# Optimization experiments

Hardware: AMD Instinct MI355X
Metric: run time of the kernel (lower is better)

The kernel has to match this reference:

```python
import jax, jax.numpy as jnp
import numpy as np

B, P, E, H = 16, 1024, 1024, 16
DH = E // H  # 64


def setup_inputs() -> dict:
    key = jax.random.key(0)
    ks = jax.random.split(key, 7)
    # kaiming_uniform on [H, DH, DH]: bound = sqrt(6 / fan_in), fan_in = DH
    bound = float(np.sqrt(6.0 / DH))
    w_att_val = jax.random.uniform(ks[0], (H, DH, DH), jnp.float32, -bound, bound)
    attention_bias = jax.random.normal(ks[1], (H, P, P), jnp.float32)
    lb = float(1.0 / np.sqrt(E))
    wv_w = jax.random.uniform(ks[2], (E, E), jnp.float32, -lb, lb)
    wv_b = jax.random.uniform(ks[3], (E,), jnp.float32, -lb, lb)
    out_w = jax.random.uniform(ks[4], (E, E), jnp.float32, -lb, lb)
    out_b = jax.random.uniform(ks[5], (E,), jnp.float32, -lb, lb)
    x = jax.random.normal(ks[6], (B, P, E), jnp.float32)
    return {"x": x, "w_att_val": w_att_val, "attention_bias": attention_bias,
            "wv_w": wv_w, "wv_b": wv_b, "out_w": out_w, "out_b": out_b}


def reference(x, w_att_val, attention_bias, wv_w, wv_b, out_w, out_b):
    b, p, e = x.shape
    dh = e // H
    # split heads: [B, H, P, DH]
    x_h = x.reshape(b, p, H, dh).transpose(0, 2, 1, 3)
    # bilinear scores: (x_h @ W) @ x_h^T -> [B, H, P, P]
    xw = jnp.einsum('bhpd,hde->bhpe', x_h, w_att_val)
    scores = jnp.einsum('bhpe,bhqe->bhpq', xw, x_h)
    scores = scores / jnp.sqrt(jnp.asarray(dh, x.dtype)) + attention_bias
    attn = jax.nn.softmax(scores, axis=-1)
    # values: Linear(E, E) then split heads
    vx = x @ wv_w.T + wv_b
    vx = vx.reshape(b, p, H, dh).transpose(0, 2, 1, 3)
    out = jnp.einsum('bhpq,bhqd->bhpd', attn, vx)
    out = out.transpose(0, 2, 1, 3).reshape(b, p, e)
    return out @ out_w.T + out_b
```

## Files before the change

### kernel.cpp

```cpp
#include <hip/hip_runtime.h>

#define PB 16
#define PP 1024
#define PE 1024
#define PH 16
#define PDH 64

typedef __attribute__((ext_vector_type(8))) short bf16x8;
typedef __attribute__((ext_vector_type(4))) short bf16x4;
typedef __attribute__((ext_vector_type(4))) float f32x4;

#define LOG2E 1.44269504088896340736f

__device__ __forceinline__ short f2bf(float f) {
    union { float f; unsigned u; } a;
    a.f = f;
    unsigned u = a.u;
    u += 0x7fffu + ((u >> 16) & 1u);
    return (short)(u >> 16);
}
__device__ __forceinline__ float bf2f(short s) {
    union { unsigned u; float f; } a;
    a.u = ((unsigned)(unsigned short)s) << 16;
    return a.f;
}
__device__ __forceinline__ unsigned cvtpk(float lo, float hi) {
    unsigned r;
    asm("v_cvt_pk_bf16_f32 %0, %1, %2" : "=v"(r) : "v"(lo), "v"(hi));
    return r;
}
union U8 { unsigned u[4]; bf16x8 v; };
__device__ __forceinline__ void async16(const void* g, void* l) {
    __builtin_amdgcn_global_load_lds(
        (const __attribute__((address_space(1))) unsigned int*)g,
        (__attribute__((address_space(3))) unsigned int*)l, 16, 0, 0);
}

__global__ __launch_bounds__(256) void wconv(const float* __restrict__ wvw,
                                             const float* __restrict__ outw,
                                             short* __restrict__ wvwb,
                                             short* __restrict__ outwb) {
    int bid = blockIdx.x;
    const float* src = (bid < 512) ? wvw : outw;
    short* dst = (bid < 512) ? wvwb : outwb;
    int lb = (bid < 512) ? bid : bid - 512;
    size_t idx = ((size_t)lb * 256 + threadIdx.x) * 8;
    float4 a = *(const float4*)(src + idx);
    float4 b = *(const float4*)(src + idx + 4);
    bf16x8 t = {f2bf(a.x), f2bf(a.y), f2bf(a.z), f2bf(a.w),
                f2bf(b.x), f2bf(b.y), f2bf(b.z), f2bf(b.w)};
    *(bf16x8*)(dst + idx) = t;
}

__global__ __launch_bounds__(256) void xw_kernel(const float* __restrict__ x,
                                                 const float* __restrict__ watt,
                                                 short* __restrict__ xw,
                                                 short* __restrict__ xbf) {
    int bid = blockIdx.x;
    int q4 = bid & 3;
    int bh = bid >> 2;
    int h = bh & 15;
    __shared__ short Wt[64][88];

    int tid = threadIdx.x;
    {
        const float* W = watt + (size_t)h * 4096;
        int idx = tid * 16;
        int d = idx >> 6, e0 = idx & 63;
#pragma unroll
        for (int i = 0; i < 16; i += 4) {
            float4 v = *(const float4*)(W + d * 64 + e0 + i);
            Wt[e0 + i + 0][d] = f2bf(v.x);
            Wt[e0 + i + 1][d] = f2bf(v.y);
            Wt[e0 + i + 2][d] = f2bf(v.z);
            Wt[e0 + i + 3][d] = f2bf(v.w);
        }
    }
    __syncthreads();

    int wave = tid >> 6, lane = tid & 63;
    int lm = lane & 15, lq = lane >> 4;

    bf16x8 bfr[4][2];
#pragma unroll
    for (int nt = 0; nt < 4; nt++)
#pragma unroll
        for (int kf = 0; kf < 2; kf++)
            bfr[nt][kf] = *(const bf16x8*)&Wt[nt * 16 + lm][kf * 32 + lq * 8];

    int b = bh >> 4;
    const float QSCALE = 0.125f * LOG2E;
    for (int pass = 0; pass < 4; pass++) {
        int p0 = q4 * 256 + pass * 64 + wave * 16;
        const float* xrow = x + ((size_t)(b * 1024 + p0 + lm)) * 1024 + h * 64;
        short* xorow = xbf + ((size_t)(b * 1024 + p0 + lm)) * 1024 + h * 64;
        bf16x8 af[2];
#pragma unroll
        for (int kf = 0; kf < 2; kf++) {
            float4 v0 = *(const float4*)(xrow + kf * 32 + lq * 8);
            float4 v1 = *(const float4*)(xrow + kf * 32 + lq * 8 + 4);
            bf16x8 t;
            t[0] = f2bf(v0.x); t[1] = f2bf(v0.y); t[2] = f2bf(v0.z); t[3] = f2bf(v0.w);
            t[4] = f2bf(v1.x); t[5] = f2bf(v1.y); t[6] = f2bf(v1.z); t[7] = f2bf(v1.w);
            af[kf] = t;
            *(bf16x8*)(xorow + kf * 32 + lq * 8) = t;
        }
#pragma unroll
        for (int nt = 0; nt < 4; nt++) {
            f32x4 acc = {0.f, 0.f, 0.f, 0.f};
            acc = __builtin_amdgcn_mfma_f32_16x16x32_bf16(af[0], bfr[nt][0], acc, 0, 0, 0);
            acc = __builtin_amdgcn_mfma_f32_16x16x32_bf16(af[1], bfr[nt][1], acc, 0, 0, 0);
            size_t base = ((size_t)bh * 1024 + p0 + lq * 4) * 64 + nt * 16 + lm;
#pragma unroll
            for (int r = 0; r < 4; r++)
                xw[base + (size_t)r * 64] = f2bf(acc[r] * QSCALE);
        }
    }
}

__global__ __launch_bounds__(256) void vx_gemm(const short* __restrict__ xbf,
                                               const short* __restrict__ wvwb,
                                               const float* __restrict__ wvb,
                                               short* __restrict__ vt) {
    int logical = (blockIdx.x & 7) * 128 + (blockIdx.x >> 3);
    int mblk = logical >> 3, nblk = logical & 7;
    int m0 = mblk * 128, n0 = nblk * 128;
    __shared__ short As[128 * 32];
    __shared__ short Bs[128 * 32];

    int tid = threadIdx.x;
    int wv = tid >> 6, ln = tid & 63;
    int c0 = wv * 2;
    int rrow = ln >> 2, rseg = (ln & 3) * 8;
    const short* gA = xbf + (size_t)(m0 + c0 * 16 + rrow) * 1024 + rseg;
    const short* gB = wvwb + (size_t)(n0 + c0 * 16 + rrow) * 1024 + rseg;
    short* lA = As + c0 * 512;
    short* lB = Bs + c0 * 512;

    int lane = ln, lm = lane & 15, lq = lane >> 4;
    int wm = (wv >> 1) * 64, wn = (wv & 1) * 64;

    f32x4 acc[4][4];
#pragma unroll
    for (int i = 0; i < 4; i++)
#pragma unroll
        for (int j = 0; j < 4; j++) acc[i][j] = (f32x4){0.f, 0.f, 0.f, 0.f};

    for (int k0 = 0; k0 < 1024; k0 += 32) {
        __syncthreads();
        async16(gA + k0, lA);
        async16(gA + k0 + 16 * 1024, lA + 512);
        async16(gB + k0, lB);
        async16(gB + k0 + 16 * 1024, lB + 512);
        __syncthreads();
        bf16x8 af[4], bfr[4];
#pragma unroll
        for (int mt = 0; mt < 4; mt++) af[mt] = *(const bf16x8*)&As[(wm + mt * 16 + lm) * 32 + lq * 8];
#pragma unroll
        for (int nt = 0; nt < 4; nt++) bfr[nt] = *(const bf16x8*)&Bs[(wn + nt * 16 + lm) * 32 + lq * 8];
#pragma unroll
        for (int mt = 0; mt < 4; mt++)
#pragma unroll
            for (int nt = 0; nt < 4; nt++)
                acc[mt][nt] = __builtin_amdgcn_mfma_f32_16x16x32_bf16(af[mt], bfr[nt], acc[mt][nt], 0, 0, 0);
    }

#pragma unroll
    for (int nt = 0; nt < 4; nt++) {
        int e = n0 + wn + nt * 16 + lm;
        float bias = wvb[e];
        int hh = e >> 6, dd = e & 63;
#pragma unroll
        for (int mt = 0; mt < 4; mt++) {
            int pg = m0 + wm + mt * 16 + lq * 4;
            int bb = pg >> 10, pp = pg & 1023;
            bf16x4 pk;
#pragma unroll
            for (int r = 0; r < 4; r++) pk[r] = f2bf(acc[mt][nt][r] + bias);
            *(bf16x4*)(vt + ((size_t)((bb * 16 + hh) * 64 + dd)) * 1024 + pp) = pk;
        }
    }
}

__global__ __launch_bounds__(256, 3) void flash_kernel(const short* __restrict__ xbf,
                                                       const short* __restrict__ xw,
                                                       const short* __restrict__ vt,
                                                       const float* __restrict__ bias,
                                                       short* __restrict__ obuf) {
    int logical = (blockIdx.x & 7) * 256 + (blockIdx.x >> 3);
    int qblk = logical & 7, b = (logical >> 3) & 15, h = logical >> 7;
    int bh = b * 16 + h;
    int q0 = qblk * 128;

    __shared__ short Ks[64][72];
    __shared__ short Vs[64][72];
    __shared__ float Rs[4][36];

    int tid = threadIdx.x, wave = tid >> 6, lane = tid & 63;
    int lm = lane & 15, lq = lane >> 4;

    bf16x8 qa[2][2];
#pragma unroll
    for (int qt = 0; qt < 2; qt++)
#pragma unroll
        for (int kf = 0; kf < 2; kf++)
            qa[qt][kf] = *(const bf16x8*)(xw + ((size_t)bh * 1024 + q0 + wave * 32 + qt * 16 + lm) * 64 + kf * 32 + lq * 8);

    f32x4 o[2][4];
#pragma unroll
    for (int qt = 0; qt < 2; qt++)
#pragma unroll
        for (int dt = 0; dt < 4; dt++) o[qt][dt] = (f32x4){0.f, 0.f, 0.f, 0.f};
    float rs[2] = {0.f, 0.f};

    int ci0 = tid * 2, ci1 = tid * 2 + 1;
    int r0 = ci0 >> 3, s0 = (ci0 & 7) * 8;
    int r1 = ci1 >> 3, s1 = (ci1 & 7) * 8;
    const short* kg = xbf + ((size_t)(b * 1024)) * 1024 + h * 64;
    const short* vg = vt + ((size_t)bh * 64) * 1024;
    const float* bg = bias + ((size_t)h << 20) + (size_t)(q0 + wave * 32) * 1024;

    bf16x8 kr[2], vr[2];
    float4 br[4][2];
    kr[0] = *(const bf16x8*)(kg + (size_t)r0 * 1024 + s0);
    kr[1] = *(const bf16x8*)(kg + (size_t)r1 * 1024 + s1);
    vr[0] = *(const bf16x8*)(vg + (size_t)r0 * 1024 + s0);
    vr[1] = *(const bf16x8*)(vg + (size_t)r1 * 1024 + s1);
#pragma unroll
    for (int kt = 0; kt < 4; kt++)
#pragma unroll
        for (int qt = 0; qt < 2; qt++)
            br[kt][qt] = *(const float4*)(bg + (size_t)(qt * 16 + lm) * 1024 + kt * 16 + lq * 4);
    *(bf16x8*)&Ks[r0][s0] = kr[0];
    *(bf16x8*)&Ks[r1][s1] = kr[1];
    *(bf16x8*)&Vs[r0][s0] = vr[0];
    *(bf16x8*)&Vs[r1][s1] = vr[1];

    for (int tile = 0; tile < 16; tile++) {
        int kv0 = tile * 64;
        __syncthreads();

        f32x4 s[4][2];
#pragma unroll
        for (int kt = 0; kt < 4; kt++)
#pragma unroll
            for (int qt = 0; qt < 2; qt++) {
                float4 bv = br[kt][qt];
                s[kt][qt] = (f32x4){bv.x * LOG2E, bv.y * LOG2E, bv.z * LOG2E, bv.w * LOG2E};
            }

        if (tile < 15) {
            int kvn = kv0 + 64;
            kr[0] = *(const bf16x8*)(kg + (size_t)(kvn + r0) * 1024 + s0);
            kr[1] = *(const bf16x8*)(kg + (size_t)(kvn + r1) * 1024 + s1);
            vr[0] = *(const bf16x8*)(vg + (size_t)r0 * 1024 + kvn + s0);
            vr[1] = *(const bf16x8*)(vg + (size_t)r1 * 1024 + kvn + s1);
#pragma unroll
            for (int kt = 0; kt < 4; kt++)
#pragma unroll
                for (int qt = 0; qt < 2; qt++)
                    br[kt][qt] = *(const float4*)(bg + (size_t)(qt * 16 + lm) * 1024 + kvn + kt * 16 + lq * 4);
        }

        __builtin_amdgcn_s_setprio(1);
#pragma unroll
        for (int kf = 0; kf < 2; kf++) {
            bf16x8 ka[4];
#pragma unroll
            for (int kt = 0; kt < 4; kt++)
                ka[kt] = *(const bf16x8*)&Ks[kt * 16 + lm][kf * 32 + lq * 8];
#pragma unroll
            for (int kt = 0; kt < 4; kt++)
#pragma unroll
                for (int qt = 0; qt < 2; qt++)
                    s[kt][qt] = __builtin_amdgcn_mfma_f32_16x16x32_bf16(ka[kt], qa[qt][kf], s[kt][qt], 0, 0, 0);
        }
        __builtin_amdgcn_s_setprio(0);

#pragma unroll
        for (int kt = 0; kt < 4; kt++)
#pragma unroll
            for (int qt = 0; qt < 2; qt++)
#pragma unroll
                for (int r = 0; r < 4; r++) {
                    float pv = __builtin_amdgcn_exp2f(s[kt][qt][r]);
                    s[kt][qt][r] = pv;
                    rs[qt] += pv;
                }

        __builtin_amdgcn_s_setprio(1);
#pragma unroll
        for (int kf = 0; kf < 2; kf++) {
            bf16x8 pa[2];
#pragma unroll
            for (int qt = 0; qt < 2; qt++) {
                U8 u;
                u.u[0] = cvtpk(s[kf * 2][qt][0], s[kf * 2][qt][1]);
                u.u[1] = cvtpk(s[kf * 2][qt][2], s[kf * 2][qt][3]);
                u.u[2] = cvtpk(s[kf * 2 + 1][qt][0], s[kf * 2 + 1][qt][1]);
                u.u[3] = cvtpk(s[kf * 2 + 1][qt][2], s[kf * 2 + 1][qt][3]);
                pa[qt] = u.v;
            }
#pragma unroll
            for (int dt = 0; dt < 4; dt++) {
                U8 uv;
                *(bf16x4*)&uv.u[0] = *(const bf16x4*)&Vs[dt * 16 + lm][kf * 32 + lq * 4];
                *(bf16x4*)&uv.u[2] = *(const bf16x4*)&Vs[dt * 16 + lm][kf * 32 + 16 + lq * 4];
#pragma unroll
                for (int qt = 0; qt < 2; qt++)
                    o[qt][dt] = __builtin_amdgcn_mfma_f32_16x16x32_bf16(pa[qt], uv.v, o[qt][dt], 0, 0, 0);
            }
        }
        __builtin_amdgcn_s_setprio(0);

        __syncthreads();
        if (tile < 15) {
            *(bf16x8*)&Ks[r0][s0] = kr[0];
            *(bf16x8*)&Ks[r1][s1] = kr[1];
            *(bf16x8*)&Vs[r0][s0] = vr[0];
            *(bf16x8*)&Vs[r1][s1] = vr[1];
        }
    }

#pragma unroll
    for (int qt = 0; qt < 2; qt++) {
        rs[qt] += __shfl_xor(rs[qt], 16);
        rs[qt] += __shfl_xor(rs[qt], 32);
    }
    if (lq == 0) { Rs[wave][lm] = rs[0]; Rs[wave][16 + lm] = rs[1]; }
    __syncthreads();

#pragma unroll
    for (int qt = 0; qt < 2; qt++) {
        float inv[4];
#pragma unroll
        for (int r = 0; r < 4; r++)
            inv[r] = 1.f / Rs[wave][qt * 16 + lq * 4 + r];
#pragma unroll
        for (int dt = 0; dt < 4; dt++) {
            int e = h * 64 + dt * 16 + lm;
#pragma unroll
            for (int r = 0; r < 4; r++) {
                int p = q0 + wave * 32 + qt * 16 + lq * 4 + r;
                obuf[((size_t)(b * 1024 + p)) * 1024 + e] = f2bf(o[qt][dt][r] * inv[r]);
            }
        }
    }
}

__global__ __launch_bounds__(256) void out_gemm(const short* __restrict__ obuf,
                                                const short* __restrict__ outwb,
                                                const float* __restrict__ outb,
                                                float* __restrict__ out) {
    int logical = (blockIdx.x & 7) * 128 + (blockIdx.x >> 3);
    int mblk = logical >> 3, nblk = logical & 7;
    int m0 = mblk * 128, n0 = nblk * 128;
    __shared__ short As[128 * 32];
    __shared__ short Bs[128 * 32];

    int tid = threadIdx.x;
    int wv = tid >> 6, ln = tid & 63;
    int c0 = wv * 2;
    int rrow = ln >> 2, rseg = (ln & 3) * 8;
    const short* gA = obuf + (size_t)(m0 + c0 * 16 + rrow) * 1024 + rseg;
    const short* gB = outwb + (size_t)(n0 + c0 * 16 + rrow) * 1024 + rseg;
    short* lA = As + c0 * 512;
    short* lB = Bs + c0 * 512;

    int lm = ln & 15, lq = ln >> 4;
    int wm = (wv >> 1) * 64, wn = (wv & 1) * 64;

    f32x4 acc[4][4];
#pragma unroll
    for (int i = 0; i < 4; i++)
#pragma unroll
        for (int j = 0; j < 4; j++) acc[i][j] = (f32x4){0.f, 0.f, 0.f, 0.f};

    for (int k0 = 0; k0 < 1024; k0 += 32) {
        __syncthreads();
        async16(gA + k0, lA);
        async16(gA + k0 + 16 * 1024, lA + 512);
        async16(gB + k0, lB);
        async16(gB + k0 + 16 * 1024, lB + 512);
        __syncthreads();
        bf16x8 af[4], bfr[4];
#pragma unroll
        for (int mt = 0; mt < 4; mt++) af[mt] = *(const bf16x8*)&As[(wm + mt * 16 + lm) * 32 + lq * 8];
#pragma unroll
        for (int nt = 0; nt < 4; nt++) bfr[nt] = *(const bf16x8*)&Bs[(wn + nt * 16 + lm) * 32 + lq * 8];
#pragma unroll
        for (int mt = 0; mt < 4; mt++)
#pragma unroll
            for (int nt = 0; nt < 4; nt++)
                acc[mt][nt] = __builtin_amdgcn_mfma_f32_16x16x32_bf16(af[mt], bfr[nt], acc[mt][nt], 0, 0, 0);
    }

#pragma unroll
    for (int nt = 0; nt < 4; nt++) {
        int e = n0 + wn + nt * 16 + lm;
        float bias = outb[e];
#pragma unroll
        for (int mt = 0; mt < 4; mt++) {
            int pg = m0 + wm + mt * 16 + lq * 4;
#pragma unroll
            for (int r = 0; r < 4; r++)
                out[(size_t)(pg + r) * 1024 + e] = acc[mt][nt][r] + bias;
        }
    }
}

extern "C" void kernel_launch(void* const* d_in, const int* in_sizes, int n_in,
                              void* d_out, int out_size, void* d_ws, size_t ws_size,
                              hipStream_t stream) {
    const float* x    = (const float*)d_in[0];
    const float* watt = (const float*)d_in[1];
    const float* bias = (const float*)d_in[2];
    const float* wvw  = (const float*)d_in[3];
    const float* wvb  = (const float*)d_in[4];
    const float* outw = (const float*)d_in[5];
    const float* outb = (const float*)d_in[6];
    float* out = (float*)d_out;

    char* ws = (char*)d_ws;
    short* xw     = (short*)ws;
    short* vt     = (short*)(ws + ((size_t)32 << 20));
    short* obuf   = (short*)(ws + ((size_t)64 << 20));
    short* xbf    = (short*)(ws + ((size_t)96 << 20));
    short* wvwb   = (short*)(ws + ((size_t)128 << 20));
    short* outwb  = (short*)(ws + ((size_t)130 << 20));

    xw_kernel<<<PB * PH * 4, 256, 0, stream>>>(x, watt, xw, xbf);
    wconv<<<1024, 256, 0, stream>>>(wvw, outw, wvwb, outwb);
    vx_gemm<<<(PB * PP / 128) * (PE / 128), 256, 0, stream>>>(xbf, wvwb, wvb, vt);
    flash_kernel<<<PB * PH * (PP / 128), 256, 0, stream>>>(xbf, xw, vt, bias, obuf);
    out_gemm<<<(PB * PP / 128) * (PE / 128), 256, 0, stream>>>(obuf, outwb, outb, out);
}
```

Baseline: 423.2 us.

## Pre-pack attention bias to bf16 in MFMA fragment layout for flash kernel

```diff
diff --git a/kernel.cpp b/kernel.cpp
--- a/kernel.cpp
+++ b/kernel.cpp
@@ -34,6 +34,37 @@
     __builtin_amdgcn_global_load_lds(
         (const __attribute__((address_space(1))) unsigned int*)g,
         (__attribute__((address_space(3))) unsigned int*)l, 16, 0, 0);
+}
+
+__global__ __launch_bounds__(256) void bias_prep(const float* __restrict__ bias,
+                                                 short* __restrict__ biasP) {
+    int bid = blockIdx.x;
+    int h = bid >> 7, qblk = (bid >> 4) & 7, tile = bid & 15;
+    int q0 = qblk * 128, kv0 = tile * 64;
+    __shared__ short T[128][68];
+
+    int t = threadIdx.x;
+    {
+        int qr = t >> 1, half = t & 1;
+        const float* src = bias + ((size_t)h << 20) + (size_t)(q0 + qr) * 1024 + kv0 + half * 32;
+#pragma unroll
+        for (int i = 0; i < 32; i += 4) {
+            float4 v = *(const float4*)(src + i);
+            bf16x4 p = {f2bf(v.x * LOG2E), f2bf(v.y * LOG2E), f2bf(v.z * LOG2E), f2bf(v.w * LOG2E)};
+            *(bf16x4*)&T[qr][half * 32 + i] = p;
+        }
+    }
+    __syncthreads();
+
+    int w = t >> 6, l = t & 63, lm = l & 15, lq = l >> 4;
+    short* dst = biasP + (((size_t)(h * 16 + tile) * 8 + qblk) * 4 + w) * 2048 + l * 8;
+#pragma unroll
+    for (int j = 0; j < 4; j++) {
+        bf16x4 a = *(const bf16x4*)&T[w * 32 + lm][j * 16 + lq * 4];
+        bf16x4 b = *(const bf16x4*)&T[w * 32 + 16 + lm][j * 16 + lq * 4];
+        bf16x8 o = {a[0], a[1], a[2], a[3], b[0], b[1], b[2], b[3]};
+        *(bf16x8*)(dst + j * 512) = o;
+    }
 }
 
 __global__ __launch_bounds__(256) void wconv(const float* __restrict__ wvw,
@@ -185,7 +216,7 @@
 __global__ __launch_bounds__(256, 3) void flash_kernel(const short* __restrict__ xbf,
                                                        const short* __restrict__ xw,
                                                        const short* __restrict__ vt,
-                                                       const float* __restrict__ bias,
+                                                       const short* __restrict__ biasP,
                                                        short* __restrict__ obuf) {
     int logical = (blockIdx.x & 7) * 256 + (blockIdx.x >> 3);
     int qblk = logical & 7, b = (logical >> 3) & 15, h = logical >> 7;
@@ -218,19 +249,18 @@
     int r1 = ci1 >> 3, s1 = (ci1 & 7) * 8;
     const short* kg = xbf + ((size_t)(b * 1024)) * 1024 + h * 64;
     const short* vg = vt + ((size_t)bh * 64) * 1024;
-    const float* bg = bias + ((size_t)h << 20) + (size_t)(q0 + wave * 32) * 1024;
+    const short* bg = biasP + (((size_t)(h * 16) * 8 + qblk) * 4 + wave) * 2048 + lane * 8;
+    const size_t BT_STRIDE = 65536;
 
     bf16x8 kr[2], vr[2];
-    float4 br[4][2];
+    bf16x8 br[4];
     kr[0] = *(const bf16x8*)(kg + (size_t)r0 * 1024 + s0);
     kr[1] = *(const bf16x8*)(kg + (size_t)r1 * 1024 + s1);
     vr[0] = *(const bf16x8*)(vg + (size_t)r0 * 1024 + s0);
     vr[1] = *(const bf16x8*)(vg + (size_t)r1 * 1024 + s1);
 #pragma unroll
     for (int kt = 0; kt < 4; kt++)
-#pragma unroll
-        for (int qt = 0; qt < 2; qt++)
-            br[kt][qt] = *(const float4*)(bg + (size_t)(qt * 16 + lm) * 1024 + kt * 16 + lq * 4);
+        br[kt] = *(const bf16x8*)(bg + kt * 512);
     *(bf16x8*)&Ks[r0][s0] = kr[0];
     *(bf16x8*)&Ks[r1][s1] = kr[1];
     *(bf16x8*)&Vs[r0][s0] = vr[0];
@@ -245,8 +275,8 @@
         for (int kt = 0; kt < 4; kt++)
 #pragma unroll
             for (int qt = 0; qt < 2; qt++) {
-                float4 bv = br[kt][qt];
-                s[kt][qt] = (f32x4){bv.x * LOG2E, bv.y * LOG2E, bv.z * LOG2E, bv.w * LOG2E};
+                s[kt][qt] = (f32x4){bf2f(br[kt][qt * 4 + 0]), bf2f(br[kt][qt * 4 + 1]),
+                                    bf2f(br[kt][qt * 4 + 2]), bf2f(br[kt][qt * 4 + 3])};
             }
 
         if (tile < 15) {
@@ -255,14 +285,12 @@
             kr[1] = *(const bf16x8*)(kg + (size_t)(kvn + r1) * 1024 + s1);
             vr[0] = *(const bf16x8*)(vg + (size_t)r0 * 1024 + kvn + s0);
             vr[1] = *(const bf16x8*)(vg + (size_t)r1 * 1024 + kvn + s1);
+            const short* bgn = bg + (size_t)(tile + 1) * BT_STRIDE;
 #pragma unroll
             for (int kt = 0; kt < 4; kt++)
-#pragma unroll
-                for (int qt = 0; qt < 2; qt++)
-                    br[kt][qt] = *(const float4*)(bg + (size_t)(qt * 16 + lm) * 1024 + kvn + kt * 16 + lq * 4);
-        }
-
-        __builtin_amdgcn_s_setprio(1);
+                br[kt] = *(const bf16x8*)(bgn + kt * 512);
+        }
+
 #pragma unroll
         for (int kf = 0; kf < 2; kf++) {
             bf16x8 ka[4];
@@ -275,7 +303,6 @@
                 for (int qt = 0; qt < 2; qt++)
                     s[kt][qt] = __builtin_amdgcn_mfma_f32_16x16x32_bf16(ka[kt], qa[qt][kf], s[kt][qt], 0, 0, 0);
         }
-        __builtin_amdgcn_s_setprio(0);
 
 #pragma unroll
         for (int kt = 0; kt < 4; kt++)
@@ -288,7 +315,6 @@
                     rs[qt] += pv;
                 }
 
-        __builtin_amdgcn_s_setprio(1);
 #pragma unroll
         for (int kf = 0; kf < 2; kf++) {
             bf16x8 pa[2];
@@ -311,7 +337,6 @@
                     o[qt][dt] = __builtin_amdgcn_mfma_f32_16x16x32_bf16(pa[qt], uv.v, o[qt][dt], 0, 0, 0);
             }
         }
-        __builtin_amdgcn_s_setprio(0);
 
         __syncthreads();
         if (tile < 15) {
@@ -426,12 +451,14 @@
     short* vt     = (short*)(ws + ((size_t)32 << 20));
     short* obuf   = (short*)(ws + ((size_t)64 << 20));
     short* xbf    = (short*)(ws + ((size_t)96 << 20));
-    short* wvwb   = (short*)(ws + ((size_t)128 << 20));
-    short* outwb  = (short*)(ws + ((size_t)130 << 20));
+    short* biasP  = (short*)(ws + ((size_t)128 << 20));
+    short* wvwb   = (short*)(ws + ((size_t)160 << 20));
+    short* outwb  = (short*)(ws + ((size_t)162 << 20));
 
     xw_kernel<<<PB * PH * 4, 256, 0, stream>>>(x, watt, xw, xbf);
+    bias_prep<<<2048, 256, 0, stream>>>(bias, biasP);
     wconv<<<1024, 256, 0, stream>>>(wvw, outw, wvwb, outwb);
     vx_gemm<<<(PB * PP / 128) * (PE / 128), 256, 0, stream>>>(xbf, wvwb, wvb, vt);
-    flash_kernel<<<PB * PH * (PP / 128), 256, 0, stream>>>(xbf, xw, vt, bias, obuf);
+    flash_kernel<<<PB * PH * (PP / 128), 256, 0, stream>>>(xbf, xw, vt, biasP, obuf);
     out_gemm<<<(PB * PP / 128) * (PE / 128), 256, 0, stream>>>(obuf, outwb, outb, out);
 }
```

New measurement: 379.3 us. -10.4%, faster.
